# Optimization experiments

Hardware: AMD Instinct MI355X
Metric: run time of the kernel (lower is better)

## Reference

```python
import jax, jax.numpy as jnp
import numpy as np

N = 50000
E = 800000
F_IN = 128
HID = 32
NEG_SLOPE = 0.2  # PyG GATConv default


def _gat_layer(x, src, dst, W, a_src, a_dst, b, heads, out_c, concat, n_nodes):
    # Linear transform per head: [N, heads, out_c]
    h = (x @ W).reshape(n_nodes, heads, out_c)
    # Per-node attention logits per head
    al_src = jnp.einsum('nhc,hc->nh', h, a_src)  # source contribution
    al_dst = jnp.einsum('nhc,hc->nh', h, a_dst)  # destination contribution
    # Edge logits (message j=src -> i=dst), leaky relu
    e = jax.nn.leaky_relu(al_src[src] + al_dst[dst], NEG_SLOPE)  # [E', heads]
    # Segment softmax over incoming edges of each destination node
    m = jax.ops.segment_max(e, dst, num_segments=n_nodes)
    ex = jnp.exp(e - m[dst])
    denom = jax.ops.segment_sum(ex, dst, num_segments=n_nodes)
    alpha = ex / denom[dst]  # [E', heads]; self-loops guarantee denom > 0
    # Weighted scatter-aggregate of source features
    msg = h[src] * alpha[:, :, None]  # [E', heads, out_c]
    out = jax.ops.segment_sum(msg, dst, num_segments=n_nodes)  # [N, heads, out_c]
    out = out.reshape(n_nodes, heads * out_c) if concat else out.mean(axis=1)
    return out + b


def setup_inputs() -> dict:
    key = jax.random.key(0)
    ks = jax.random.split(key, 10)
    x = jax.random.normal(ks[0], (N, F_IN), dtype=jnp.float32)
    edge_index = jax.random.randint(ks[1], (2, E), 0, N, dtype=jnp.int64)
    s = 0.1
    return {
        'x': x,
        'edge_index': edge_index,
        'W1': jax.random.normal(ks[2], (F_IN, 4 * HID), dtype=jnp.float32) * s,
        'a_src1': jax.random.normal(ks[3], (4, HID), dtype=jnp.float32) * s,
        'a_dst1': jax.random.normal(ks[4], (4, HID), dtype=jnp.float32) * s,
        'b1': jnp.zeros((4 * HID,), jnp.float32),
        'W2': jax.random.normal(ks[5], (4 * HID, 2 * HID), dtype=jnp.float32) * s,
        'a_src2': jax.random.normal(ks[6], (2, HID), dtype=jnp.float32) * s,
        'a_dst2': jax.random.normal(ks[7], (2, HID), dtype=jnp.float32) * s,
        'b2': jnp.zeros((2 * HID,), jnp.float32),
        'W3': jax.random.normal(ks[8], (2 * HID, 1), dtype=jnp.float32) * s,
        'a_src3': jax.random.normal(ks[9], (1, 1), dtype=jnp.float32) * s,
        'a_dst3': jax.random.normal(jax.random.fold_in(key, 99), (1, 1), dtype=jnp.float32) * s,
        'b3': jnp.zeros((1,), jnp.float32),
    }


def reference(x, edge_index, W1, a_src1, a_dst1, b1, W2, a_src2, a_dst2, b2, W3, a_src3, a_dst3, b3):
    n = x.shape[0]
    # add_self_loops=True (PyG default)
    loop = jnp.arange(n, dtype=edge_index.dtype)
    src = jnp.concatenate([edge_index[0], loop])
    dst = jnp.concatenate([edge_index[1], loop])
    h = _gat_layer(x, src, dst, W1, a_src1, a_dst1, b1, 4, HID, True, n)
    h = jax.nn.elu(h)  # dropout is identity in eval mode
    h = _gat_layer(h, src, dst, W2, a_src2, a_dst2, b2, 2, HID, True, n)
    h = jax.nn.elu(h)
    out = _gat_layer(h, src, dst, W3, a_src3, a_dst3, b3, 1, 1, False, n)
    return out  # [N, 1]
```

## Files before the change

### kernel.cpp

```cpp
#include <hip/hip_runtime.h>
#include <hip/hip_fp16.h>
#include <math.h>

#define F_IN 128
constexpr int SB = 256;
constexpr float LOG2E = 1.4426950408889634f;
constexpr int CAP = 131072;
constexpr int CHUNK = 4096;

__global__ void scan1(const int* __restrict__ in, int* __restrict__ out,
                      int* __restrict__ bsums, int n, int selfN) {
    __shared__ int sm[SB];
    int i = blockIdx.x * SB + threadIdx.x;
    int v = (i < n) ? (in[i] + (i < selfN ? 1 : 0)) : 0;
    sm[threadIdx.x] = v;
    __syncthreads();
    for (int d = 1; d < SB; d <<= 1) {
        int t = (threadIdx.x >= d) ? sm[threadIdx.x - d] : 0;
        __syncthreads();
        sm[threadIdx.x] += t;
        __syncthreads();
    }
    if (i < n) out[i] = sm[threadIdx.x] - v;
    if (threadIdx.x == SB - 1) bsums[blockIdx.x] = sm[SB - 1];
}

__global__ void scan2(int* __restrict__ bsums, int nb) {
    __shared__ int sm[SB];
    int v = (threadIdx.x < nb) ? bsums[threadIdx.x] : 0;
    sm[threadIdx.x] = v;
    __syncthreads();
    for (int d = 1; d < SB; d <<= 1) {
        int t = (threadIdx.x >= d) ? sm[threadIdx.x - d] : 0;
        __syncthreads();
        sm[threadIdx.x] += t;
        __syncthreads();
    }
    if (threadIdx.x < nb) bsums[threadIdx.x] = sm[threadIdx.x] - v;
}

__global__ void scan3(int* __restrict__ off, int* __restrict__ cursor,
                      const int* __restrict__ bsums, int n, int ncur) {
    int i = blockIdx.x * SB + threadIdx.x;
    if (i < n) {
        int v = off[i] + bsums[blockIdx.x];
        off[i] = v;
        if (i < ncur) cursor[i] = v;
    }
}

template <int BN, int TN, int HEADS, typename AT>
__device__ __forceinline__ void gemm_dev(
    const AT* __restrict__ A, const float* __restrict__ B,
    const float* __restrict__ asrc, const float* __restrict__ adst,
    __half* __restrict__ C, float* __restrict__ als, float* __restrict__ ald,
    int M, int bid, char* smem) {
    constexpr int BM = 128, BK = 16, TM = 4, K = 128;
    float (*As)[BM + 4] = (float (*)[BM + 4])smem;
    float (*Bs)[BN] = (float (*)[BN])(smem + (size_t)BK * (BM + 4) * 4);
    const int tx = threadIdx.x, ty = threadIdx.y;
    const int tid = ty * 16 + tx;
    const int row0 = bid * BM;
    const int i0 = ty * TM;
    const int j0a = tx * 4;
    const int j0b = 64 + tx * 4;

    float acc[TM][TN];
#pragma unroll
    for (int m = 0; m < TM; ++m)
#pragma unroll
        for (int n = 0; n < TN; ++n) acc[m][n] = 0.f;

    const int ar = tid >> 2;
    const int ak = (tid & 3) * 4;
    int arow = row0 + ar;
    if (arow >= M) arow = M - 1;
    const AT* Aptr = A + (size_t)arow * K + ak;
    const int bk = (BN == 128) ? (tid >> 5) : (tid >> 4);
    const int bc = (BN == 128) ? ((tid & 31) * 4) : ((tid & 15) * 4);
    const bool bact = (BN == 128) || (tid < 256);

    for (int kc = 0; kc < K; kc += BK) {
        float a0, a1v, a2v, a3v;
        if constexpr (sizeof(AT) == 4) {
            float4 av = *(const float4*)(Aptr + kc);
            a0 = av.x; a1v = av.y; a2v = av.z; a3v = av.w;
        } else {
            uint2 raw = *(const uint2*)(Aptr + kc);
            __half2 h01 = *(__half2*)&raw.x;
            __half2 h23 = *(__half2*)&raw.y;
            float2 f01 = __half22float2(h01);
            float2 f23 = __half22float2(h23);
            a0 = f01.x; a1v = f01.y; a2v = f23.x; a3v = f23.y;
        }
        float4 bv;
        if (bact) bv = *(const float4*)(B + (size_t)(kc + bk) * BN + bc);
        __syncthreads();
        As[ak + 0][ar] = a0;
        As[ak + 1][ar] = a1v;
        As[ak + 2][ar] = a2v;
        As[ak + 3][ar] = a3v;
        if (bact) *(float4*)&Bs[bk][bc] = bv;
        __syncthreads();
#pragma unroll
        for (int kk = 0; kk < BK; ++kk) {
            float4 a4 = *(const float4*)&As[kk][i0];
            float arr[TM] = {a4.x, a4.y, a4.z, a4.w};
            float br[TN];
            float4 b0 = *(const float4*)&Bs[kk][j0a];
            br[0] = b0.x; br[1] = b0.y; br[2] = b0.z; br[3] = b0.w;
            if constexpr (TN == 8) {
                float4 b1 = *(const float4*)&Bs[kk][j0b];
                br[4] = b1.x; br[5] = b1.y; br[6] = b1.z; br[7] = b1.w;
            }
#pragma unroll
            for (int m = 0; m < TM; ++m)
#pragma unroll
                for (int n = 0; n < TN; ++n) acc[m][n] += arr[m] * br[n];
        }
    }

#pragma unroll
    for (int m = 0; m < TM; ++m) {
        int row = row0 + i0 + m;
        bool ok = row < M;
        if constexpr (TN == 8) {
            if (ok) {
                alignas(8) __half2 pa[2], pb[2];
#pragma unroll
                for (int n2 = 0; n2 < 2; ++n2) {
                    pa[n2] = __floats2half2_rn(acc[m][2 * n2], acc[m][2 * n2 + 1]);
                    pb[n2] = __floats2half2_rn(acc[m][4 + 2 * n2], acc[m][5 + 2 * n2]);
                }
                *(uint2*)&C[(size_t)row * BN + j0a] = *(uint2*)pa;
                *(uint2*)&C[(size_t)row * BN + j0b] = *(uint2*)pb;
            }
            float psA = 0.f, pdA = 0.f, psB = 0.f, pdB = 0.f;
#pragma unroll
            for (int n = 0; n < 4; ++n) {
                psA += acc[m][n] * asrc[j0a + n];
                pdA += acc[m][n] * adst[j0a + n];
                psB += acc[m][n + 4] * asrc[j0b + n];
                pdB += acc[m][n + 4] * adst[j0b + n];
            }
#pragma unroll
            for (int msk = 1; msk < 8; msk <<= 1) {
                psA += __shfl_xor(psA, msk, 64);
                pdA += __shfl_xor(pdA, msk, 64);
                psB += __shfl_xor(psB, msk, 64);
                pdB += __shfl_xor(pdB, msk, 64);
            }
            if (ok && (tx & 7) == 0) {
                int hA = tx >> 3;
                als[row * HEADS + hA] = psA * LOG2E;
                ald[row * HEADS + hA] = pdA * LOG2E;
                als[row * HEADS + 2 + hA] = psB * LOG2E;
                ald[row * HEADS + 2 + hA] = pdB * LOG2E;
            }
        } else {
            if (ok) {
                alignas(8) __half2 ph[2];
#pragma unroll
                for (int n2 = 0; n2 < 2; ++n2)
                    ph[n2] = __floats2half2_rn(acc[m][2 * n2], acc[m][2 * n2 + 1]);
                *(uint2*)&C[(size_t)row * BN + j0a] = *(uint2*)ph;
            }
            float ps = 0.f, pd = 0.f;
#pragma unroll
            for (int n = 0; n < TN; ++n) {
                ps += acc[m][n] * asrc[j0a + n];
                pd += acc[m][n] * adst[j0a + n];
            }
#pragma unroll
            for (int msk = 1; msk < 8; msk <<= 1) {
                ps += __shfl_xor(ps, msk, 64);
                pd += __shfl_xor(pd, msk, 64);
            }
            if (ok && (tx & 7) == 0) {
                int h0 = tx >> 3;
                als[row * HEADS + h0] = ps * LOG2E;
                ald[row * HEADS + h0] = pd * LOG2E;
            }
        }
    }
}

__global__ __launch_bounds__(512) void gemm1_bucket(
    const float* __restrict__ A, const float* __restrict__ B,
    const float* __restrict__ asrc, const float* __restrict__ adst,
    __half* __restrict__ C, float* __restrict__ als, float* __restrict__ ald,
    int M, int gblk,
    const int* __restrict__ src, const int* __restrict__ dst,
    int* __restrict__ deg, int* __restrict__ bucketcur,
    int2* __restrict__ ebuf, int E, int nspan, int nchunk) {
    __shared__ __align__(16) char smem[CHUNK * 8 + 32 * 4];
    if ((int)blockIdx.x < gblk) {
        gemm_dev<128, 8, 4, float>(A, B, asrc, adst, C, als, ald, M, blockIdx.x, smem);
        return;
    }
    int cid = blockIdx.x - gblk;
    if (cid >= nchunk) return;
    int tid = threadIdx.y * 16 + threadIdx.x;
    int2* stage = (int2*)smem;
    int* hist = (int*)(smem + CHUNK * 8);
    int* bbase = hist + 8;
    int* gbase = hist + 16;
    if (tid < 8) hist[tid] = 0;
    __syncthreads();
    int ebase = cid * CHUNK;
    int s[8], d[8], bk[8], slot[8];
#pragma unroll
    for (int k = 0; k < 8; ++k) {
        int e = ebase + k * 512 + tid;
        bool v = e < E;
        s[k] = v ? src[e] : 0;
        d[k] = v ? dst[e] : 0;
        bk[k] = -1;
        if (v) {
            bk[k] = d[k] / nspan;
            slot[k] = atomicAdd(&hist[bk[k]], 1);
            atomicAdd(&deg[d[k]], 1);
        }
    }
    __syncthreads();
    if (tid == 0) {
        int run = 0;
#pragma unroll
        for (int b = 0; b < 8; ++b) { bbase[b] = run; run += hist[b]; }
    }
    if (tid < 8) gbase[tid] = atomicAdd(&bucketcur[tid], hist[tid]);
    __syncthreads();
#pragma unroll
    for (int k = 0; k < 8; ++k)
        if (bk[k] >= 0) stage[bbase[bk[k]] + slot[k]] = make_int2(s[k], d[k]);
    __syncthreads();
    for (int b = 0; b < 8; ++b) {
        int c0 = bbase[b], cN = hist[b];
        size_t g0 = (size_t)b * CAP + gbase[b];
        for (int j = tid; j < cN; j += 512) ebuf[g0 + j] = stage[c0 + j];
    }
}

__global__ void scatter_b(const int2* __restrict__ ebuf,
                          const int* __restrict__ bucketcur,
                          int* __restrict__ cursor, unsigned short* __restrict__ csr,
                          int N, int nspan, int spb) {
    int g = blockIdx.x & 7;
    int c = blockIdx.x >> 3;
    int tid = threadIdx.x;
    int cnt = bucketcur[g];
    const int2* eb = ebuf + (size_t)g * CAP;
    int stride = spb * 256;
    for (int i = c * 256 + tid; i < cnt; i += stride) {
        int2 e = eb[i];
        int p = atomicAdd(&cursor[e.y], 1);
        csr[p] = (unsigned short)e.x;
    }
    int r0 = g * nspan, r1 = r0 + nspan;
    if (r1 > N) r1 = N;
    for (int i = r0 + c * 256 + tid; i < r1; i += stride) {
        int p = atomicAdd(&cursor[i], 1);
        csr[p] = (unsigned short)i;
    }
}

template <int BN, int TN, int HEADS>
__global__ __launch_bounds__(512) void gemm_fused_h(
    const __half* __restrict__ A, const float* __restrict__ B,
    const float* __restrict__ asrc, const float* __restrict__ adst,
    __half* __restrict__ C, float* __restrict__ als, float* __restrict__ ald,
    int M) {
    __shared__ __align__(16) char smem[16 * 132 * 4 + 16 * BN * 4];
    gemm_dev<BN, TN, HEADS, __half>(A, B, asrc, adst, C, als, ald, M, blockIdx.x, smem);
}

__global__ void gat_agg_l1(const __half* __restrict__ h,
                           const float* __restrict__ als, const float* __restrict__ ald,
                           const float* __restrict__ bias,
                           const int* __restrict__ off,
                           const unsigned short* __restrict__ csr,
                           __half* __restrict__ out, int n) {
    int wid = (blockIdx.x * blockDim.x + threadIdx.x) >> 6;
    int lane = threadIdx.x & 63;
    if (wid >= n) return;
    const int g = lane >> 4;
    const int q = lane & 15;
    const int hd = q >> 2;
    float ad = ald[wid * 4 + hd];
    int e0 = off[wid], e1 = off[wid + 1];
    const __half* hq = h + q * 8;

    float acc[8] = {0.f, 0.f, 0.f, 0.f, 0.f, 0.f, 0.f, 0.f};
    float D = 0.f;

    auto LD = [&](int ebase, uint4& h4, float& al) {
        int ee = ebase + g;
        int ie = (ee < e1) ? ee : e1 - 1;
        int s = csr[ie];
        float av = als[s * 4 + hd];
        al = (ee < e1) ? av : -1e30f;
        h4 = *(const uint4*)(hq + (size_t)s * 128);
    };
    auto PROC = [&](const uint4& h4, float al) {
        float lg = al + ad;
        lg = fmaxf(lg, 0.2f * lg);
        float exv = exp2f(lg);
        D += exv;
        const __half2* hh = (const __half2*)&h4;
#pragma unroll
        for (int i = 0; i < 4; ++i) {
            float2 f = __half22float2(hh[i]);
            acc[2 * i] = fmaf(exv, f.x, acc[2 * i]);
            acc[2 * i + 1] = fmaf(exv, f.y, acc[2 * i + 1]);
        }
    };

    uint4 hA, hB;
    float alA, alB;
    LD(e0, hA, alA);
    LD(e0 + 4, hB, alB);
    int e = e0;
    for (; e + 8 < e1; e += 8) {
        uint4 nA, nB;
        float nalA, nalB;
        LD(e + 8, nA, nalA);
        LD(e + 12, nB, nalB);
        PROC(hA, alA);
        PROC(hB, alB);
        hA = nA; alA = nalA;
        hB = nB; alB = nalB;
    }
    PROC(hA, alA);
    PROC(hB, alB);

#pragma unroll
    for (int i = 0; i < 8; ++i) {
        acc[i] += __shfl_xor(acc[i], 16, 64);
        acc[i] += __shfl_xor(acc[i], 32, 64);
    }
    D += __shfl_xor(D, 16, 64);
    D += __shfl_xor(D, 32, 64);

    if (g == 0) {
        float inv = 1.f / D;
        alignas(16) __half2 ph[4];
#pragma unroll
        for (int i = 0; i < 4; ++i) {
            float2 bv = ((const float2*)bias)[q * 4 + i];
            float vx = acc[2 * i] * inv + bv.x;
            float vy = acc[2 * i + 1] * inv + bv.y;
            vx = vx > 0.f ? vx : (__expf(vx) - 1.f);
            vy = vy > 0.f ? vy : (__expf(vy) - 1.f);
            ph[i] = __floats2half2_rn(vx, vy);
        }
        *(uint4*)(out + (size_t)wid * 128 + q * 8) = *(uint4*)ph;
    }
}

__global__ void gat_agg_l2(const __half* __restrict__ h,
                           const float* __restrict__ als, const float* __restrict__ ald,
                           const float* __restrict__ bias,
                           const int* __restrict__ off,
                           const unsigned short* __restrict__ csr,
                           const float* __restrict__ W3, const float* __restrict__ as3,
                           const float* __restrict__ ad3, float2* __restrict__ hs,
                           float* __restrict__ ald3, int n) {
    int wid = (blockIdx.x * blockDim.x + threadIdx.x) >> 6;
    int lane = threadIdx.x & 63;
    if (wid >= n) return;
    const int g = lane >> 3;
    const int q = lane & 7;
    const int hd = q >> 2;
    float ad = ald[wid * 2 + hd];
    int e0 = off[wid], e1 = off[wid + 1];
    const __half* hq = h + q * 8;

    float acc[8] = {0.f, 0.f, 0.f, 0.f, 0.f, 0.f, 0.f, 0.f};
    float D = 0.f;

    auto LD = [&](int ebase, uint4& h4, float& al) {
        int ee = ebase + g;
        int ie = (ee < e1) ? ee : e1 - 1;
        int s = csr[ie];
        float av = als[s * 2 + hd];
        al = (ee < e1) ? av : -1e30f;
        h4 = *(const uint4*)(hq + (size_t)s * 64);
    };
    auto PROC = [&](const uint4& h4, float al) {
        float lg = al + ad;
        lg = fmaxf(lg, 0.2f * lg);
        float exv = exp2f(lg);
        D += exv;
        const __half2* hh = (const __half2*)&h4;
#pragma unroll
        for (int i = 0; i < 4; ++i) {
            float2 f = __half22float2(hh[i]);
            acc[2 * i] = fmaf(exv, f.x, acc[2 * i]);
            acc[2 * i + 1] = fmaf(exv, f.y, acc[2 * i + 1]);
        }
    };

    uint4 hA, hB;
    float alA, alB;
    LD(e0, hA, alA);
    LD(e0 + 8, hB, alB);
    int e = e0;
    for (; e + 16 < e1; e += 16) {
        uint4 nA, nB;
        float nalA, nalB;
        LD(e + 16, nA, nalA);
        LD(e + 24, nB, nalB);
        PROC(hA, alA);
        PROC(hB, alB);
        hA = nA; alA = nalA;
        hB = nB; alB = nalB;
    }
    PROC(hA, alA);
    PROC(hB, alB);

#pragma unroll
    for (int i = 0; i < 8; ++i) {
        acc[i] += __shfl_xor(acc[i], 8, 64);
        acc[i] += __shfl_xor(acc[i], 16, 64);
        acc[i] += __shfl_xor(acc[i], 32, 64);
    }
    D += __shfl_xor(D, 8, 64);
    D += __shfl_xor(D, 16, 64);
    D += __shfl_xor(D, 32, 64);

    float inv = 1.f / D;
    float r = 0.f;
#pragma unroll
    for (int i = 0; i < 8; ++i) {
        float v = acc[i] * inv + bias[q * 8 + i];
        v = v > 0.f ? v : (__expf(v) - 1.f);
        r = fmaf(v, W3[q * 8 + i], r);
    }
#pragma unroll
    for (int msk = 1; msk < 8; msk <<= 1) r += __shfl_xor(r, msk, 64);
    if (lane == 0) {
        hs[wid] = make_float2(r, r * as3[0] * LOG2E);
        ald3[wid] = r * ad3[0] * LOG2E;
    }
}

__global__ void gat_agg1(const float2* __restrict__ hs, const float* __restrict__ ald3,
                         const float* __restrict__ bias,
                         const int* __restrict__ off,
                         const unsigned short* __restrict__ csr,
                         float* __restrict__ out, int n) {
    int i = blockIdx.x * blockDim.x + threadIdx.x;
    if (i >= n) return;
    float ad = ald3[i];
    int e0 = off[i], e1 = off[i + 1];
    float S = 0.f, D = 0.f;
    float2 g[2];
    float valid[2];
#pragma unroll
    for (int p = 0; p < 2; ++p) {
        int ee = e0 + p;
        int ie = (ee < e1) ? ee : e1 - 1;
        int s = csr[ie];
        g[p] = hs[s];
        valid[p] = (ee < e1) ? 0.f : -1e30f;
    }
    int e = e0;
    for (; e + 2 < e1; e += 2) {
#pragma unroll
        for (int p = 0; p < 2; ++p) {
            int ee = e + 2 + p;
            int ie = (ee < e1) ? ee : e1 - 1;
            int s = csr[ie];
            float2 ng = hs[s];
            float nvalid = (ee < e1) ? 0.f : -1e30f;
            float lg = g[p].y + ad + valid[p];
            lg = fmaxf(lg, 0.2f * lg);
            float exv = exp2f(lg);
            D += exv;
            S = fmaf(exv, g[p].x, S);
            g[p] = ng;
            valid[p] = nvalid;
        }
    }
#pragma unroll
    for (int p = 0; p < 2; ++p) {
        float lg = g[p].y + ad + valid[p];
        lg = fmaxf(lg, 0.2f * lg);
        float exv = exp2f(lg);
        D += exv;
        S = fmaf(exv, g[p].x, S);
    }
    out[i] = S / D + bias[0];
}

extern "C" void kernel_launch(void* const* d_in, const int* in_sizes, int n_in,
                              void* d_out, int out_size, void* d_ws, size_t ws_size,
                              hipStream_t stream) {
    const float* x   = (const float*)d_in[0];
    const int*   ei  = (const int*)d_in[1];
    const float* W1  = (const float*)d_in[2];
    const float* as1 = (const float*)d_in[3];
    const float* ad1 = (const float*)d_in[4];
    const float* b1  = (const float*)d_in[5];
    const float* W2  = (const float*)d_in[6];
    const float* as2 = (const float*)d_in[7];
    const float* ad2 = (const float*)d_in[8];
    const float* b2  = (const float*)d_in[9];
    const float* W3  = (const float*)d_in[10];
    const float* as3 = (const float*)d_in[11];
    const float* ad3 = (const float*)d_in[12];
    const float* b3  = (const float*)d_in[13];
    float* out = (float*)d_out;

    const int N = in_sizes[0] / F_IN;
    const int E = in_sizes[1] / 2;
    const int ET = E + N;

    char* w = (char*)d_ws;
    size_t o = 0;
    auto alloc = [&](size_t bytes) -> void* {
        void* p = w + o;
        o += (bytes + 255) & ~(size_t)255;
        return p;
    };
    __half* hbuf = (__half*)alloc((size_t)N * 128 * 2);
    __half* a1   = (__half*)alloc((size_t)N * 128 * 2);
    float2* hs   = (float2*)alloc((size_t)N * 8);
    float* als  = (float*)alloc((size_t)N * 4 * 4);
    float* ald  = (float*)alloc((size_t)N * 4 * 4);
    float* ald3 = (float*)alloc((size_t)N * 4);
    int* deg    = (int*)alloc((size_t)(N + 1) * 4);
    int* bucketcur = (int*)alloc(8 * 4);
    int* off    = (int*)alloc((size_t)(N + 1) * 4);
    int* cursor = (int*)alloc((size_t)N * 4);
    int* bsums  = (int*)alloc(1024);
    unsigned short* csr = (unsigned short*)alloc((size_t)ET * 2);
    int2* ebuf  = (int2*)alloc((size_t)8 * CAP * 8);

    __half* h2 = hbuf;

    const int* esrc = ei;
    const int* edst = ei + E;
    const int nspan = (N + 7) >> 3;
    const int nchunk = (E + CHUNK - 1) / CHUNK;

    hipMemsetAsync(deg, 0, (size_t)(N + 1) * 4, stream);
    hipMemsetAsync(bucketcur, 0, 8 * 4, stream);

    const int gblk = (N + 127) / 128;

    gemm1_bucket<<<gblk + nchunk, dim3(16, 32), 0, stream>>>(
        x, W1, as1, ad1, hbuf, als, ald, N, gblk,
        esrc, edst, deg, bucketcur, ebuf, E, nspan, nchunk);

    int n1 = N + 1;
    int nb = (n1 + SB - 1) / SB;
    scan1<<<nb, SB, 0, stream>>>(deg, off, bsums, n1, N);
    scan2<<<1, SB, 0, stream>>>(bsums, nb);
    scan3<<<nb, SB, 0, stream>>>(off, cursor, bsums, n1, N);

    {
        const int spb = 32;
        scatter_b<<<8 * spb, 256, 0, stream>>>(ebuf, bucketcur, cursor, csr, N, nspan, spb);
    }

    gat_agg_l1<<<(N * 64 + 255) / 256, 256, 0, stream>>>(
        hbuf, als, ald, b1, off, csr, a1, N);

    gemm_fused_h<64, 4, 2><<<gblk, dim3(16, 32), 0, stream>>>(
        a1, W2, as2, ad2, h2, als, ald, N);
    gat_agg_l2<<<(N * 64 + 255) / 256, 256, 0, stream>>>(
        h2, als, ald, b2, off, csr, W3, as3, ad3, hs, ald3, N);

    gat_agg1<<<(N + 255) / 256, 256, 0, stream>>>(hs, ald3, b3, off, csr, out, N);
}
```

Before: 183.1 us.

## Build CSR per bucket in LDS, replacing global degree atomics and scan kernels

The global degree histogram, the three-kernel prefix scan and the global-cursor scatter are replaced by one build_csr kernel. It runs 8 blocks of 1024 threads, one per destination bucket, and each block counts degrees, scans them and scatters edges using LDS atomics. This removes the global atomics, the memset of the degree array and several kernel launches. It also halves the edge chunk size so the bucketing blocks fit in the GEMM's shared memory. The risk is that only 8 blocks do all the CSR work, which leaves most of the GPU idle during that phase, and the LDS array size is hardcoded for nspan of 6250 or less.

Measured after the change: 225.9 us. +23.4%, slower.

```diff
diff --git a/kernel.cpp b/kernel.cpp
--- a/kernel.cpp
+++ b/kernel.cpp
@@ -3,51 +3,10 @@
 #include <math.h>
 
 #define F_IN 128
-constexpr int SB = 256;
 constexpr float LOG2E = 1.4426950408889634f;
 constexpr int CAP = 131072;
-constexpr int CHUNK = 4096;
-
-__global__ void scan1(const int* __restrict__ in, int* __restrict__ out,
-                      int* __restrict__ bsums, int n, int selfN) {
-    __shared__ int sm[SB];
-    int i = blockIdx.x * SB + threadIdx.x;
-    int v = (i < n) ? (in[i] + (i < selfN ? 1 : 0)) : 0;
-    sm[threadIdx.x] = v;
-    __syncthreads();
-    for (int d = 1; d < SB; d <<= 1) {
-        int t = (threadIdx.x >= d) ? sm[threadIdx.x - d] : 0;
-        __syncthreads();
-        sm[threadIdx.x] += t;
-        __syncthreads();
-    }
-    if (i < n) out[i] = sm[threadIdx.x] - v;
-    if (threadIdx.x == SB - 1) bsums[blockIdx.x] = sm[SB - 1];
-}
-
-__global__ void scan2(int* __restrict__ bsums, int nb) {
-    __shared__ int sm[SB];
-    int v = (threadIdx.x < nb) ? bsums[threadIdx.x] : 0;
-    sm[threadIdx.x] = v;
-    __syncthreads();
-    for (int d = 1; d < SB; d <<= 1) {
-        int t = (threadIdx.x >= d) ? sm[threadIdx.x - d] : 0;
-        __syncthreads();
-        sm[threadIdx.x] += t;
-        __syncthreads();
-    }
-    if (threadIdx.x < nb) bsums[threadIdx.x] = sm[threadIdx.x] - v;
-}
-
-__global__ void scan3(int* __restrict__ off, int* __restrict__ cursor,
-                      const int* __restrict__ bsums, int n, int ncur) {
-    int i = blockIdx.x * SB + threadIdx.x;
-    if (i < n) {
-        int v = off[i] + bsums[blockIdx.x];
-        off[i] = v;
-        if (i < ncur) cursor[i] = v;
-    }
-}
+constexpr int CHUNK = 2048;
+constexpr int GEMM_SMEM = 16 * 132 * 4 + 16 * 128 * 4;
 
 template <int BN, int TN, int HEADS, typename AT>
 __device__ __forceinline__ void gemm_dev(
@@ -191,9 +150,9 @@
     __half* __restrict__ C, float* __restrict__ als, float* __restrict__ ald,
     int M, int gblk,
     const int* __restrict__ src, const int* __restrict__ dst,
-    int* __restrict__ deg, int* __restrict__ bucketcur,
-    int2* __restrict__ ebuf, int E, int nspan, int nchunk) {
-    __shared__ __align__(16) char smem[CHUNK * 8 + 32 * 4];
+    int* __restrict__ bucketcur, int2* __restrict__ ebuf,
+    int E, int nspan, int nchunk) {
+    __shared__ __align__(16) char smem[GEMM_SMEM];
     if ((int)blockIdx.x < gblk) {
         gemm_dev<128, 8, 4, float>(A, B, asrc, adst, C, als, ald, M, blockIdx.x, smem);
         return;
@@ -208,9 +167,9 @@
     if (tid < 8) hist[tid] = 0;
     __syncthreads();
     int ebase = cid * CHUNK;
-    int s[8], d[8], bk[8], slot[8];
-#pragma unroll
-    for (int k = 0; k < 8; ++k) {
+    int s[4], d[4], bk[4], slot[4];
+#pragma unroll
+    for (int k = 0; k < 4; ++k) {
         int e = ebase + k * 512 + tid;
         bool v = e < E;
         s[k] = v ? src[e] : 0;
@@ -219,7 +178,6 @@
         if (v) {
             bk[k] = d[k] / nspan;
             slot[k] = atomicAdd(&hist[bk[k]], 1);
-            atomicAdd(&deg[d[k]], 1);
         }
     }
     __syncthreads();
@@ -231,7 +189,7 @@
     if (tid < 8) gbase[tid] = atomicAdd(&bucketcur[tid], hist[tid]);
     __syncthreads();
 #pragma unroll
-    for (int k = 0; k < 8; ++k)
+    for (int k = 0; k < 4; ++k)
         if (bk[k] >= 0) stage[bbase[bk[k]] + slot[k]] = make_int2(s[k], d[k]);
     __syncthreads();
     for (int b = 0; b < 8; ++b) {
@@ -241,26 +199,75 @@
     }
 }
 
-__global__ void scatter_b(const int2* __restrict__ ebuf,
-                          const int* __restrict__ bucketcur,
-                          int* __restrict__ cursor, unsigned short* __restrict__ csr,
-                          int N, int nspan, int spb) {
-    int g = blockIdx.x & 7;
-    int c = blockIdx.x >> 3;
+__global__ __launch_bounds__(1024) void build_csr(
+    const int2* __restrict__ ebuf, const int* __restrict__ bucketcur,
+    int* __restrict__ off, unsigned short* __restrict__ csr, int N, int nspan) {
+    __shared__ int S[6272];
+    __shared__ int wsum[16];
+    int g = blockIdx.x;
     int tid = threadIdx.x;
+    int r0 = g * nspan;
+    int r1 = r0 + nspan; if (r1 > N) r1 = N;
+    int nloc = r1 - r0;
     int cnt = bucketcur[g];
     const int2* eb = ebuf + (size_t)g * CAP;
-    int stride = spb * 256;
-    for (int i = c * 256 + tid; i < cnt; i += stride) {
+    int base = 0;
+    for (int gg = 0; gg < g; ++gg) {
+        int rr0 = gg * nspan;
+        int rr1 = rr0 + nspan; if (rr1 > N) rr1 = N;
+        base += bucketcur[gg] + (rr1 - rr0);
+    }
+    for (int i = tid; i < nloc; i += 1024) S[i] = 0;
+    __syncthreads();
+    for (int i = tid; i < cnt; i += 1024) atomicAdd(&S[eb[i].y - r0], 1);
+    __syncthreads();
+    constexpr int EPT = 7;
+    int lo = tid * EPT;
+    int vals[EPT];
+    int tot = 0;
+#pragma unroll
+    for (int k = 0; k < EPT; ++k) {
+        int i = lo + k;
+        int v = (i < nloc) ? S[i] + 1 : 0;
+        vals[k] = tot;
+        tot += v;
+    }
+    int lane = tid & 63;
+    int wv = tid >> 6;
+    int run = tot;
+    for (int dd = 1; dd < 64; dd <<= 1) {
+        int t = __shfl_up(run, dd, 64);
+        if (lane >= dd) run += t;
+    }
+    if (lane == 63) wsum[wv] = run;
+    __syncthreads();
+    if (wv == 0) {
+        int v = (lane < 16) ? wsum[lane] : 0;
+        int r = v;
+        for (int dd = 1; dd < 64; dd <<= 1) {
+            int t = __shfl_up(r, dd, 64);
+            if (lane >= dd) r += t;
+        }
+        if (lane < 16) wsum[lane] = r - v;
+    }
+    __syncthreads();
+    int texcl = (run - tot) + wsum[wv];
+#pragma unroll
+    for (int k = 0; k < EPT; ++k) {
+        int i = lo + k;
+        if (i < nloc) {
+            int sstart = texcl + vals[k];
+            off[r0 + i] = base + sstart;
+            csr[base + sstart] = (unsigned short)(r0 + i);
+            S[i] = sstart + 1;
+        }
+    }
+    if (g == 7 && tid == 0) off[N] = base + cnt + nloc;
+    __syncthreads();
+    for (int i = tid; i < cnt; i += 1024) {
         int2 e = eb[i];
-        int p = atomicAdd(&cursor[e.y], 1);
-        csr[p] = (unsigned short)e.x;
-    }
-    int r0 = g * nspan, r1 = r0 + nspan;
-    if (r1 > N) r1 = N;
-    for (int i = r0 + c * 256 + tid; i < r1; i += stride) {
-        int p = atomicAdd(&cursor[i], 1);
-        csr[p] = (unsigned short)i;
+        int p = atomicAdd(&S[e.y - r0], 1);
+        csr[base + p] = (unsigned short)e.x;
     }
 }
 
@@ -529,11 +536,8 @@
     float* als  = (float*)alloc((size_t)N * 4 * 4);
     float* ald  = (float*)alloc((size_t)N * 4 * 4);
     float* ald3 = (float*)alloc((size_t)N * 4);
-    int* deg    = (int*)alloc((size_t)(N + 1) * 4);
     int* bucketcur = (int*)alloc(8 * 4);
     int* off    = (int*)alloc((size_t)(N + 1) * 4);
-    int* cursor = (int*)alloc((size_t)N * 4);
-    int* bsums  = (int*)alloc(1024);
     unsigned short* csr = (unsigned short*)alloc((size_t)ET * 2);
     int2* ebuf  = (int2*)alloc((size_t)8 * CAP * 8);
 
@@ -544,25 +548,15 @@
     const int nspan = (N + 7) >> 3;
     const int nchunk = (E + CHUNK - 1) / CHUNK;
 
-    hipMemsetAsync(deg, 0, (size_t)(N + 1) * 4, stream);
     hipMemsetAsync(bucketcur, 0, 8 * 4, stream);
 
     const int gblk = (N + 127) / 128;
 
     gemm1_bucket<<<gblk + nchunk, dim3(16, 32), 0, stream>>>(
         x, W1, as1, ad1, hbuf, als, ald, N, gblk,
-        esrc, edst, deg, bucketcur, ebuf, E, nspan, nchunk);
-
-    int n1 = N + 1;
-    int nb = (n1 + SB - 1) / SB;
-    scan1<<<nb, SB, 0, stream>>>(deg, off, bsums, n1, N);
-    scan2<<<1, SB, 0, stream>>>(bsums, nb);
-    scan3<<<nb, SB, 0, stream>>>(off, cursor, bsums, n1, N);
-
-    {
-        const int spb = 32;
-        scatter_b<<<8 * spb, 256, 0, stream>>>(ebuf, bucketcur, cursor, csr, N, nspan, spb);
-    }
+        esrc, edst, bucketcur, ebuf, E, nspan, nchunk);
+
+    build_csr<<<8, 1024, 0, stream>>>(ebuf, bucketcur, off, csr, N, nspan);
 
     gat_agg_l1<<<(N * 64 + 255) / 256, 256, 0, stream>>>(
         hbuf, als, ald, b1, off, csr, a1, N);
```
